# Optimization experiments

Hardware: AMD Instinct MI355X
Metric: run time of the kernel (lower is better)

## Reference

```python
import jax, jax.numpy as jnp
import numpy as np

B, C, H, W = 8, 64, 256, 256


def setup_inputs() -> dict:
    key = jax.random.key(0)
    ks = jax.random.split(key, 7)
    return {
        "x": jax.random.normal(ks[0], (B, C, H, W), dtype=jnp.float32),
        "query_w": jax.random.normal(ks[1], (C, W, W), dtype=jnp.float32),
        "key_w": jax.random.normal(ks[2], (C, W, W), dtype=jnp.float32),
        "var_w": jax.random.normal(ks[3], (C, W, W), dtype=jnp.float32),
        "query_b": jax.random.normal(ks[4], (C, H, W), dtype=jnp.float32),
        "key_b": jax.random.normal(ks[5], (C, H, W), dtype=jnp.float32),
        "var_b": jax.random.normal(ks[6], (C, H, W), dtype=jnp.float32),
    }


def reference(x, query_w, key_w, var_w, query_b, key_b, var_b):
    # mode == 'horizontal': per-channel right-matmul over the W axis.
    # x: [B,C,H,W], *_w: [C,W,W] (broadcast over batch), *_b: [C,H,W].
    q = jnp.einsum("bchw,cwv->bchv", x, query_w) + query_b
    k = jnp.einsum("bchw,cwv->bchv", x, key_w) + key_b
    v = jnp.einsum("bchw,cwv->bchv", x, var_w) + var_b
    return jax.nn.softmax(q * k, axis=-1) * v
```

## Files before the change

### kernel.cpp

```cpp
#include <hip/hip_runtime.h>
#include <math.h>


#define Bn 8
#define Cn 64
#define Hn 256
#define Wn 256

typedef _Float16 f16x8 __attribute__((ext_vector_type(8)));
typedef _Float16 f16x4 __attribute__((ext_vector_type(4)));
typedef float    f32x16 __attribute__((ext_vector_type(16)));

#define MFMA(a, b, c) __builtin_amdgcn_mfma_f32_32x32x16_f16((a), (b), (c), 0, 0, 0)

#define LDS_ALO 2048
#define LDS_B   4096
#define LDS_SM  36864

__global__ __launch_bounds__(512, 4) void axile_attn_mfma4(
    const float* __restrict__ x,
    const float* __restrict__ wq,
    const float* __restrict__ wk,
    const float* __restrict__ wv,
    const float* __restrict__ bq,
    const float* __restrict__ bk,
    const float* __restrict__ bv,
    float* __restrict__ out)
{
    __shared__ __align__(16) char lds[39424];

    const int tid  = threadIdx.x;
    const int ncol = tid >> 6;
    const int lane = tid & 63;
    const int h    = lane >> 5;
    const int l31  = lane & 31;

    const int blk = blockIdx.x;
    const int c   = blk & 63;
    const int j   = blk >> 6;
    const int b   = j >> 2;
    const int h0  = (j & 3) * 64;

    const float* xbase = x + ((size_t)(b * Cn + c) * Hn + h0) * Wn;
    const float* w_q = wq + (size_t)c * Wn * Wn;
    const float* w_k = wk + (size_t)c * Wn * Wn;
    const float* w_v = wv + (size_t)c * Wn * Wn;

    const int wkh = tid >> 8;
    const int n   = tid & 255;
    const int ntW = n >> 5;
    const int nl  = n & 31;
    const int wfo = ((wkh << 5) | nl) * 16;
    const int am    = tid >> 2;
    const int akq   = tid & 3;
    const int amt   = am >> 5;
    const int alc   = ((akq >> 1) << 5) | (am & 31);
    const int aboff = (akq & 1) * 8;

    f32x16 accq[2], acck[2];
#pragma unroll
    for (int mt = 0; mt < 2; ++mt)
#pragma unroll
        for (int r = 0; r < 16; ++r) {
            accq[mt][r] = 0.f;
            acck[mt][r] = 0.f;
        }

    for (int kt = 0; kt < 16; ++kt) {
        const int k0 = kt * 16;
        __syncthreads();
#pragma unroll
        for (int mat = 0; mat < 2; ++mat) {
            const float* Wp = mat ? w_k : w_q;
            const float* wrow = Wp + (size_t)(k0 + wkh * 8) * Wn + n;
            float w8[8];
#pragma unroll
            for (int r = 0; r < 8; ++r)
                w8[r] = wrow[(size_t)r * Wn];
            f16x8 hi8, lo8;
#pragma unroll
            for (int e = 0; e < 8; ++e) {
                const float wv_ = w8[e];
                _Float16 hv = (_Float16)wv_;
                hi8[e] = hv;
                lo8[e] = (_Float16)(wv_ - (float)hv);
            }
            char* dplane = lds + LDS_B + (mat * 2) * 8192 + ntW * 1024;
            *(f16x8*)(dplane + wfo) = hi8;
            *(f16x8*)(dplane + 8192 + wfo) = lo8;
        }
        if (tid < 256) {
            const float4 xx = *(const float4*)(xbase + (size_t)am * Wn + k0 + akq * 4);
            f16x4 hi4, lo4;
            _Float16 t0 = (_Float16)xx.x; hi4[0] = t0; lo4[0] = (_Float16)(xx.x - (float)t0);
            _Float16 t1 = (_Float16)xx.y; hi4[1] = t1; lo4[1] = (_Float16)(xx.y - (float)t1);
            _Float16 t2 = (_Float16)xx.z; hi4[2] = t2; lo4[2] = (_Float16)(xx.z - (float)t2);
            _Float16 t3 = (_Float16)xx.w; hi4[3] = t3; lo4[3] = (_Float16)(xx.w - (float)t3);
            *(f16x4*)(lds + amt * 1024 + alc * 16 + aboff) = hi4;
            *(f16x4*)(lds + LDS_ALO + amt * 1024 + alc * 16 + aboff) = lo4;
        }
        __syncthreads();

        f16x8 ah[2], al[2];
#pragma unroll
        for (int mt = 0; mt < 2; ++mt) {
            ah[mt] = *(const f16x8*)(lds + mt * 1024 + lane * 16);
            al[mt] = *(const f16x8*)(lds + LDS_ALO + mt * 1024 + lane * 16);
        }
        const char* bb = lds + LDS_B + ncol * 1024 + lane * 16;
        f16x8 bqh = *(const f16x8*)(bb + 0 * 8192);
        f16x8 bql = *(const f16x8*)(bb + 1 * 8192);
        f16x8 bkh = *(const f16x8*)(bb + 2 * 8192);
        f16x8 bkl = *(const f16x8*)(bb + 3 * 8192);
#pragma unroll
        for (int mt = 0; mt < 2; ++mt) {
            accq[mt] = MFMA(ah[mt], bqh, accq[mt]);
            accq[mt] = MFMA(al[mt], bqh, accq[mt]);
            accq[mt] = MFMA(ah[mt], bql, accq[mt]);
            acck[mt] = MFMA(ah[mt], bkh, acck[mt]);
            acck[mt] = MFMA(al[mt], bkh, acck[mt]);
            acck[mt] = MFMA(ah[mt], bkl, acck[mt]);
        }
    }

    float* part    = (float*)(lds + LDS_SM);
    float* combmax = (float*)(lds + LDS_SM + 2048);
    float* combsum = (float*)(lds + LDS_SM + 2304);

#pragma unroll
    for (int mt = 0; mt < 2; ++mt)
#pragma unroll
        for (int r = 0; r < 16; ++r) {
            const int rl = (r & 3) + 8 * (r >> 2) + 4 * h;
            const int hh = h0 + mt * 32 + rl;
            const int vv = ncol * 32 + l31;
            const size_t bidx = ((size_t)c * Hn + hh) * Wn + vv;
            const float qv = accq[mt][r] + bq[bidx];
            const float kv = acck[mt][r] + bk[bidx];
            accq[mt][r] = qv * kv;
        }

#pragma unroll
    for (int mt = 0; mt < 2; ++mt)
#pragma unroll
        for (int r = 0; r < 16; ++r) {
            float m2 = accq[mt][r];
#pragma unroll
            for (int off = 16; off > 0; off >>= 1)
                m2 = fmaxf(m2, __shfl_xor(m2, off, 64));
            if ((lane & 15) == r && ((lane >> 4) & 1) == mt) {
                const int rl  = (r & 3) + 8 * (r >> 2) + 4 * h;
                const int row = mt * 32 + rl;
                part[ncol * 64 + row] = m2;
            }
        }
    __syncthreads();
    if (tid < 64) {
        float m = part[tid];
#pragma unroll
        for (int w = 1; w < 8; ++w)
            m = fmaxf(m, part[w * 64 + tid]);
        combmax[tid] = m;
    }
    __syncthreads();

#pragma unroll
    for (int mt = 0; mt < 2; ++mt)
#pragma unroll
        for (int r = 0; r < 16; ++r) {
            const int rl  = (r & 3) + 8 * (r >> 2) + 4 * h;
            const int row = mt * 32 + rl;
            const float mx = combmax[row];
            const float e0 = __expf(accq[mt][r] - mx);
            accq[mt][r] = e0;
            float ps = e0;
#pragma unroll
            for (int off = 16; off > 0; off >>= 1)
                ps += __shfl_xor(ps, off, 64);
            if ((lane & 15) == r && ((lane >> 4) & 1) == mt)
                part[ncol * 64 + row] = ps;
        }
    __syncthreads();
    if (tid < 64) {
        float s = part[tid];
#pragma unroll
        for (int w = 1; w < 8; ++w)
            s += part[w * 64 + tid];
        combsum[tid] = s;
    }

    f32x16 accv[2];
#pragma unroll
    for (int mt = 0; mt < 2; ++mt)
#pragma unroll
        for (int r = 0; r < 16; ++r)
            accv[mt][r] = 0.f;

    for (int kt = 0; kt < 16; ++kt) {
        const int k0 = kt * 16;
        __syncthreads();
        {
            const float* wrow = w_v + (size_t)(k0 + wkh * 8) * Wn + n;
            float w8[8];
#pragma unroll
            for (int r = 0; r < 8; ++r)
                w8[r] = wrow[(size_t)r * Wn];
            f16x8 hi8;
#pragma unroll
            for (int e = 0; e < 8; ++e)
                hi8[e] = (_Float16)w8[e];
            *(f16x8*)(lds + LDS_B + ntW * 1024 + wfo) = hi8;
        }
        if (tid < 256) {
            const float4 xx = *(const float4*)(xbase + (size_t)am * Wn + k0 + akq * 4);
            f16x4 hi4;
            hi4[0] = (_Float16)xx.x;
            hi4[1] = (_Float16)xx.y;
            hi4[2] = (_Float16)xx.z;
            hi4[3] = (_Float16)xx.w;
            *(f16x4*)(lds + amt * 1024 + alc * 16 + aboff) = hi4;
        }
        __syncthreads();

        f16x8 ah[2];
#pragma unroll
        for (int mt = 0; mt < 2; ++mt)
            ah[mt] = *(const f16x8*)(lds + mt * 1024 + lane * 16);
        f16x8 bvh = *(const f16x8*)(lds + LDS_B + ncol * 1024 + lane * 16);
#pragma unroll
        for (int mt = 0; mt < 2; ++mt)
            accv[mt] = MFMA(ah[mt], bvh, accv[mt]);
    }

    float* obase = out + ((size_t)(b * Cn + c) * Hn) * Wn;
#pragma unroll
    for (int mt = 0; mt < 2; ++mt)
#pragma unroll
        for (int r = 0; r < 16; ++r) {
            const int rl  = (r & 3) + 8 * (r >> 2) + 4 * h;
            const int row = mt * 32 + rl;
            const float inv = 1.0f / combsum[row];
            const int hh = h0 + row;
            const int vv = ncol * 32 + l31;
            const size_t bidx = ((size_t)c * Hn + hh) * Wn + vv;
            const float vx = accv[mt][r] + bv[bidx];
            obase[(size_t)hh * Wn + vv] = accq[mt][r] * vx * inv;
        }
}

extern "C" void kernel_launch(void* const* d_in, const int* in_sizes, int n_in,
                              void* d_out, int out_size, void* d_ws, size_t ws_size,
                              hipStream_t stream) {
    (void)in_sizes; (void)n_in; (void)out_size; (void)d_ws; (void)ws_size;
    const float* x  = (const float*)d_in[0];
    const float* wq = (const float*)d_in[1];
    const float* wk = (const float*)d_in[2];
    const float* wv = (const float*)d_in[3];
    const float* bq = (const float*)d_in[4];
    const float* bk = (const float*)d_in[5];
    const float* bv = (const float*)d_in[6];
    float* out = (float*)d_out;

    dim3 grid(Bn * 4 * Cn);
    dim3 block(512);
    hipLaunchKernelGGL(axile_attn_mfma4, grid, block, 0, stream,
                       x, wq, wk, wv, bq, bk, bv, out);
}
```

Measured before the change: 530.2 us.

## Precompute split-fp16 weight fragments in workspace and stream them via direct LDS loads

Adds a prep kernel that converts the q/k/v weights once per call into MFMA-ready fp16 hi/lo fragment planes in the workspace. The main kernel then pulls these into LDS with global_load_lds instead of re-loading and re-splitting fp32 weights in each of the 8×4 blocks per channel. Block-to-(batch, row) mapping is also changed so that blocks sharing a channel's weights run closer together, which should improve cache reuse. This adds a second launch, needs about 42 MB of workspace, and keeps the old kernel as a fallback.

```diff
diff --git a/kernel.cpp b/kernel.cpp
--- a/kernel.cpp
+++ b/kernel.cpp
@@ -16,6 +16,267 @@
 #define LDS_ALO 2048
 #define LDS_B   4096
 #define LDS_SM  36864
+
+#define WS_PLANE_H 4096
+#define WS_NEED ((size_t)Cn * 16 * 5 * 8192)
+
+__device__ __forceinline__ void ldst16(const void* g, void* l) {
+    __builtin_amdgcn_global_load_lds(
+        (const __attribute__((address_space(1))) unsigned int*)g,
+        (__attribute__((address_space(3))) unsigned int*)l, 16, 0, 0);
+}
+
+__global__ __launch_bounds__(256) void prep_w(
+    const float* __restrict__ wq, const float* __restrict__ wk,
+    const float* __restrict__ wv, _Float16* __restrict__ wf)
+{
+    const int blk = blockIdx.x;
+    const int kt  = blk & 15;
+    const int c   = blk >> 4;
+    const int n   = threadIdx.x;
+    const int ntile = n >> 5;
+    const int nl    = n & 31;
+
+    _Float16* base = wf + (size_t)blk * 5 * WS_PLANE_H;
+    const size_t woff = ((size_t)c * Wn + kt * 16) * Wn + n;
+
+#pragma unroll
+    for (int mat = 0; mat < 2; ++mat) {
+        const float* Wp = (mat ? wk : wq) + woff;
+        float w16[16];
+#pragma unroll
+        for (int r = 0; r < 16; ++r)
+            w16[r] = Wp[(size_t)r * Wn];
+        _Float16* hip = base + (mat * 2) * WS_PLANE_H + ntile * 512;
+        _Float16* lop = hip + WS_PLANE_H;
+#pragma unroll
+        for (int h2 = 0; h2 < 2; ++h2) {
+            f16x8 hi8, lo8;
+#pragma unroll
+            for (int e = 0; e < 8; ++e) {
+                const float wv_ = w16[h2 * 8 + e];
+                _Float16 hv = (_Float16)wv_;
+                hi8[e] = hv;
+                lo8[e] = (_Float16)(wv_ - (float)hv);
+            }
+            *(f16x8*)(hip + (h2 * 32 + nl) * 8) = hi8;
+            *(f16x8*)(lop + (h2 * 32 + nl) * 8) = lo8;
+        }
+    }
+    {
+        const float* Wp = wv + woff;
+        float w16[16];
+#pragma unroll
+        for (int r = 0; r < 16; ++r)
+            w16[r] = Wp[(size_t)r * Wn];
+        _Float16* vp = base + 4 * WS_PLANE_H + ntile * 512;
+#pragma unroll
+        for (int h2 = 0; h2 < 2; ++h2) {
+            f16x8 hi8;
+#pragma unroll
+            for (int e = 0; e < 8; ++e)
+                hi8[e] = (_Float16)w16[h2 * 8 + e];
+            *(f16x8*)(vp + (h2 * 32 + nl) * 8) = hi8;
+        }
+    }
+}
+
+__global__ __launch_bounds__(512, 4) void axile_attn_mfma5(
+    const float* __restrict__ x,
+    const _Float16* __restrict__ wf,
+    const float* __restrict__ bq,
+    const float* __restrict__ bk,
+    const float* __restrict__ bv,
+    float* __restrict__ out)
+{
+    __shared__ __align__(16) char lds[39424];
+
+    const int tid  = threadIdx.x;
+    const int ncol = tid >> 6;
+    const int lane = tid & 63;
+    const int h    = lane >> 5;
+    const int l31  = lane & 31;
+
+    const int blk = blockIdx.x;
+    const int c   = blk & 63;
+    const int j   = blk >> 6;
+    const int b   = j & 7;
+    const int h0  = (j >> 3) * 64;
+
+    const float* xbase = x + ((size_t)(b * Cn + c) * Hn + h0) * Wn;
+    const _Float16* wfc = wf + (size_t)c * 16 * 5 * WS_PLANE_H;
+
+    const int am    = tid >> 2;
+    const int akq   = tid & 3;
+    const int amt   = am >> 5;
+    const int alc   = ((akq >> 1) << 5) | (am & 31);
+    const int aboff = (akq & 1) * 8;
+
+    f32x16 accq[2], acck[2];
+#pragma unroll
+    for (int mt = 0; mt < 2; ++mt)
+#pragma unroll
+        for (int r = 0; r < 16; ++r) {
+            accq[mt][r] = 0.f;
+            acck[mt][r] = 0.f;
+        }
+
+    for (int kt = 0; kt < 16; ++kt) {
+        const int k0 = kt * 16;
+        const _Float16* wsp = wfc + (size_t)kt * 5 * WS_PLANE_H;
+        __syncthreads();
+#pragma unroll
+        for (int p = 0; p < 4; ++p)
+            ldst16(wsp + p * WS_PLANE_H + tid * 8,
+                   lds + LDS_B + p * 8192 + tid * 16);
+        if (tid < 256) {
+            const float4 xx = *(const float4*)(xbase + (size_t)am * Wn + k0 + akq * 4);
+            f16x4 hi4, lo4;
+            _Float16 t0 = (_Float16)xx.x; hi4[0] = t0; lo4[0] = (_Float16)(xx.x - (float)t0);
+            _Float16 t1 = (_Float16)xx.y; hi4[1] = t1; lo4[1] = (_Float16)(xx.y - (float)t1);
+            _Float16 t2 = (_Float16)xx.z; hi4[2] = t2; lo4[2] = (_Float16)(xx.z - (float)t2);
+            _Float16 t3 = (_Float16)xx.w; hi4[3] = t3; lo4[3] = (_Float16)(xx.w - (float)t3);
+            *(f16x4*)(lds + amt * 1024 + alc * 16 + aboff) = hi4;
+            *(f16x4*)(lds + LDS_ALO + amt * 1024 + alc * 16 + aboff) = lo4;
+        }
+        __syncthreads();
+
+        f16x8 ah[2], al[2];
+#pragma unroll
+        for (int mt = 0; mt < 2; ++mt) {
+            ah[mt] = *(const f16x8*)(lds + mt * 1024 + lane * 16);
+            al[mt] = *(const f16x8*)(lds + LDS_ALO + mt * 1024 + lane * 16);
+        }
+        const char* bb = lds + LDS_B + ncol * 1024 + lane * 16;
+        f16x8 bqh = *(const f16x8*)(bb + 0 * 8192);
+        f16x8 bql = *(const f16x8*)(bb + 1 * 8192);
+        f16x8 bkh = *(const f16x8*)(bb + 2 * 8192);
+        f16x8 bkl = *(const f16x8*)(bb + 3 * 8192);
+#pragma unroll
+        for (int mt = 0; mt < 2; ++mt) {
+            accq[mt] = MFMA(ah[mt], bqh, accq[mt]);
+            accq[mt] = MFMA(al[mt], bqh, accq[mt]);
+            accq[mt] = MFMA(ah[mt], bql, accq[mt]);
+            acck[mt] = MFMA(ah[mt], bkh, acck[mt]);
+            acck[mt] = MFMA(al[mt], bkh, acck[mt]);
+            acck[mt] = MFMA(ah[mt], bkl, acck[mt]);
+        }
+    }
+
+    float* part    = (float*)(lds + LDS_SM);
+    float* combmax = (float*)(lds + LDS_SM + 2048);
+    float* combsum = (float*)(lds + LDS_SM + 2304);
+
+#pragma unroll
+    for (int mt = 0; mt < 2; ++mt)
+#pragma unroll
+        for (int r = 0; r < 16; ++r) {
+            const int rl = (r & 3) + 8 * (r >> 2) + 4 * h;
+            const int hh = h0 + mt * 32 + rl;
+            const int vv = ncol * 32 + l31;
+            const size_t bidx = ((size_t)c * Hn + hh) * Wn + vv;
+            const float qv = accq[mt][r] + bq[bidx];
+            const float kv = acck[mt][r] + bk[bidx];
+            accq[mt][r] = qv * kv;
+        }
+
+#pragma unroll
+    for (int mt = 0; mt < 2; ++mt)
+#pragma unroll
+        for (int r = 0; r < 16; ++r) {
+            float m2 = accq[mt][r];
+#pragma unroll
+            for (int off = 16; off > 0; off >>= 1)
+                m2 = fmaxf(m2, __shfl_xor(m2, off, 64));
+            if ((lane & 15) == r && ((lane >> 4) & 1) == mt) {
+                const int rl  = (r & 3) + 8 * (r >> 2) + 4 * h;
+                const int row = mt * 32 + rl;
+                part[ncol * 64 + row] = m2;
+            }
+        }
+    __syncthreads();
+    if (tid < 64) {
+        float m = part[tid];
+#pragma unroll
+        for (int w = 1; w < 8; ++w)
+            m = fmaxf(m, part[w * 64 + tid]);
+        combmax[tid] = m;
+    }
+    __syncthreads();
+
+#pragma unroll
+    for (int mt = 0; mt < 2; ++mt)
+#pragma unroll
+        for (int r = 0; r < 16; ++r) {
+            const int rl  = (r & 3) + 8 * (r >> 2) + 4 * h;
+            const int row = mt * 32 + rl;
+            const float mx = combmax[row];
+            const float e0 = __expf(accq[mt][r] - mx);
+            accq[mt][r] = e0;
+            float ps = e0;
+#pragma unroll
+            for (int off = 16; off > 0; off >>= 1)
+                ps += __shfl_xor(ps, off, 64);
+            if ((lane & 15) == r && ((lane >> 4) & 1) == mt)
+                part[ncol * 64 + row] = ps;
+        }
+    __syncthreads();
+    if (tid < 64) {
+        float s = part[tid];
+#pragma unroll
+        for (int w = 1; w < 8; ++w)
+            s += part[w * 64 + tid];
+        combsum[tid] = s;
+    }
+
+    f32x16 accv[2];
+#pragma unroll
+    for (int mt = 0; mt < 2; ++mt)
+#pragma unroll
+        for (int r = 0; r < 16; ++r)
+            accv[mt][r] = 0.f;
+
+    for (int kt = 0; kt < 16; ++kt) {
+        const int k0 = kt * 16;
+        const _Float16* wsp = wfc + ((size_t)kt * 5 + 4) * WS_PLANE_H;
+        __syncthreads();
+        ldst16(wsp + tid * 8, lds + LDS_B + tid * 16);
+        if (tid < 256) {
+            const float4 xx = *(const float4*)(xbase + (size_t)am * Wn + k0 + akq * 4);
+            f16x4 hi4;
+            hi4[0] = (_Float16)xx.x;
+            hi4[1] = (_Float16)xx.y;
+            hi4[2] = (_Float16)xx.z;
+            hi4[3] = (_Float16)xx.w;
+            *(f16x4*)(lds + amt * 1024 + alc * 16 + aboff) = hi4;
+        }
+        __syncthreads();
+
+        f16x8 ah[2];
+#pragma unroll
+        for (int mt = 0; mt < 2; ++mt)
+            ah[mt] = *(const f16x8*)(lds + mt * 1024 + lane * 16);
+        f16x8 bvh = *(const f16x8*)(lds + LDS_B + ncol * 1024 + lane * 16);
+#pragma unroll
+        for (int mt = 0; mt < 2; ++mt)
+            accv[mt] = MFMA(ah[mt], bvh, accv[mt]);
+    }
+
+    float* obase = out + ((size_t)(b * Cn + c) * Hn) * Wn;
+#pragma unroll
+    for (int mt = 0; mt < 2; ++mt)
+#pragma unroll
+        for (int r = 0; r < 16; ++r) {
+            const int rl  = (r & 3) + 8 * (r >> 2) + 4 * h;
+            const int row = mt * 32 + rl;
+            const float inv = 1.0f / combsum[row];
+            const int hh = h0 + row;
+            const int vv = ncol * 32 + l31;
+            const size_t bidx = ((size_t)c * Hn + hh) * Wn + vv;
+            const float vx = accv[mt][r] + bv[bidx];
+            obase[(size_t)hh * Wn + vv] = accq[mt][r] * vx * inv;
+        }
+}
 
 __global__ __launch_bounds__(512, 4) void axile_attn_mfma4(
     const float* __restrict__ x,
@@ -38,8 +299,8 @@
     const int blk = blockIdx.x;
     const int c   = blk & 63;
     const int j   = blk >> 6;
-    const int b   = j >> 2;
-    const int h0  = (j & 3) * 64;
+    const int b   = j & 7;
+    const int h0  = (j >> 3) * 64;
 
     const float* xbase = x + ((size_t)(b * Cn + c) * Hn + h0) * Wn;
     const float* w_q = wq + (size_t)c * Wn * Wn;
@@ -251,7 +512,7 @@
 extern "C" void kernel_launch(void* const* d_in, const int* in_sizes, int n_in,
                               void* d_out, int out_size, void* d_ws, size_t ws_size,
                               hipStream_t stream) {
-    (void)in_sizes; (void)n_in; (void)out_size; (void)d_ws; (void)ws_size;
+    (void)in_sizes; (void)n_in; (void)out_size;
     const float* x  = (const float*)d_in[0];
     const float* wq = (const float*)d_in[1];
     const float* wk = (const float*)d_in[2];
@@ -261,8 +522,13 @@
     const float* bv = (const float*)d_in[6];
     float* out = (float*)d_out;
 
-    dim3 grid(Bn * 4 * Cn);
-    dim3 block(512);
-    hipLaunchKernelGGL(axile_attn_mfma4, grid, block, 0, stream,
-                       x, wq, wk, wv, bq, bk, bv, out);
+    if (d_ws != nullptr && ws_size >= WS_NEED) {
+        hipLaunchKernelGGL(prep_w, dim3(Cn * 16), dim3(256), 0, stream,
+                           wq, wk, wv, (_Float16*)d_ws);
+        hipLaunchKernelGGL(axile_attn_mfma5, dim3(Bn * 4 * Cn), dim3(512), 0, stream,
+                           x, (const _Float16*)d_ws, bq, bk, bv, out);
+    } else {
+        hipLaunchKernelGGL(axile_attn_mfma4, dim3(Bn * 4 * Cn), dim3(512), 0, stream,
+                           x, wq, wk, wv, bq, bk, bv, out);
+    }
 }
```

Result: slower. 654.8 us (+23.5%).
